# Kernel optimization log

Measured on AMD Instinct MI355X. Metric: run time of the kernel, lower is better.

The kernel has to match this reference:

```python
import math
import jax, jax.numpy as jnp
import numpy as np

B, T, H, E = 2, 1024, 8, 64
M = 128   # nb_features
W = 64    # local_context
NEG = -1e24

def _gaussian_orthogonal(m, d, rng):
    # Orthogonal random features (ortho_scaling=0: rows scaled by chi norms)
    blocks = []
    for _ in range(math.ceil(m / d)):
        q, _ = np.linalg.qr(rng.standard_normal((d, d)))
        blocks.append(q.T)
    mat = np.concatenate(blocks, 0)[:m]
    multiplier = np.linalg.norm(rng.standard_normal((m, d)), axis=1)
    return (multiplier[:, None] * mat).astype(np.float32)

def setup_inputs() -> dict:
    key = jax.random.key(0)
    kq, kk, kv = jax.random.split(key, 3)
    rng = np.random.default_rng(0)
    return {
        'query': jax.random.normal(kq, (B, T, H, E), jnp.float32),
        'key':   jax.random.normal(kk, (B, T, H, E), jnp.float32),
        'value': jax.random.normal(kv, (B, T, H, E), jnp.float32),
        'projection_matrix': jnp.asarray(_gaussian_orthogonal(M, E, rng)),
    }

def _performer_features(x, proj, is_query, temp):
    # x: (b,h,s,e), proj: (m,e). FAVOR+ positive softmax features with
    # the stabilizer returned separately as a log scale.
    normalizer = math.sqrt(temp)
    data_dash = jnp.einsum('bhse,me->bhsm', normalizer * x, proj)
    diag = 0.5 * temp * jnp.sum(x * x, axis=-1, keepdims=True)
    log_feat = data_dash - diag                      # (b,h,s,m)
    if is_query:
        stab = jax.lax.stop_gradient(jnp.max(log_feat, axis=-1, keepdims=True))      # (b,h,s,1)
    else:
        stab = jax.lax.stop_gradient(jnp.max(log_feat, axis=(-2, -1), keepdims=True))  # (b,h,1,1)
    prime = (M ** -0.5) * jnp.exp(log_feat - stab)
    return prime, stab

def reference(query, key, value, projection_matrix):
    q = jnp.transpose(query, (0, 2, 1, 3))   # (b,h,t,e)
    k = jnp.transpose(key, (0, 2, 1, 3))
    v = jnp.transpose(value, (0, 2, 1, 3))
    temp = 1.0 / math.sqrt(E)

    q_prime, q_log_scale = _performer_features(q, projection_matrix, True, temp)
    k_prime, k_log_scale = _performer_features(k, projection_matrix, False, temp)
    prime_log_scale = q_log_scale + k_log_scale        # (b,h,t,1)

    # low-rank Performer terms (non-causal linear attention)
    qk1 = jnp.einsum('bhtm,bhm->bht', q_prime, k_prime.sum(axis=2))
    kv = jnp.einsum('bhsm,bhsd->bhmd', k_prime, v)
    qkv = jnp.einsum('bhtm,bhmd->bhtd', q_prime, kv)

    # banded local attention: query t attends keys t - W//2 + j, j in [0,W)
    local_idx = jnp.arange(T)[:, None] - W // 2 + jnp.arange(W)[None, :]  # (t,w)
    valid = (local_idx >= 0) & (local_idx < T)
    cidx = jnp.clip(local_idx, 0, T - 1)

    k_win = jnp.take(k, cidx, axis=2)                  # (b,h,t,w,e)
    QK = temp * jnp.einsum('bhte,bhtwe->bhtw', q, k_win)
    QK = jnp.where(valid, QK, NEG)

    kp_win = jnp.take(k_prime, cidx, axis=2)           # (b,h,t,w,m)
    dots_prime = jnp.einsum('bhtm,bhtwm->bhtw', q_prime, kp_win)
    dots_prime = jnp.where(valid, dots_prime, 0.0)

    # log-space normalization combining exact local mass and low-rank remainder
    QK_lse = jax.nn.logsumexp(QK, axis=-1, keepdims=True)
    dps = dots_prime.sum(axis=-1, keepdims=True)
    lr_log_norm = jnp.log(jnp.clip(qk1[..., None] - dps, 1e-24, None)) + prime_log_scale
    log_norm = jnp.logaddexp(QK_lse, lr_log_norm)
    prime_scale = jnp.exp(prime_log_scale - log_norm)
    dots = jnp.exp(QK - log_norm) - dots_prime * prime_scale  # (b,h,t,w)

    v_win = jnp.take(v, cidx, axis=2)                  # (b,h,t,w,d)
    out_local = jnp.einsum('bhtw,bhtwd->bhtd', dots, v_win)
    out = out_local + qkv * prime_scale
    return jnp.transpose(out, (0, 2, 1, 3))            # (b,t,h,d)
```

## Files before the change

kernel.cpp:

```cpp
#include <hip/hip_runtime.h>

#define TT 1024
#define HH 8
#define EE 64
#define MM 128
#define NBH 16

#define NORMALIZER 0.35355339059327379f
#define RSQRT_M    0.08838834764831845f
#define TEMP       0.125f
#define NEGINF     -1e24f

typedef __attribute__((ext_vector_type(8))) short short8v;
typedef __attribute__((ext_vector_type(4))) float f32x4;
#define MFMA_BF16 __builtin_amdgcn_mfma_f32_16x16x32_bf16

#define OFF_QP    0u
#define OFF_KF    8388608u
#define OFF_KVP   16777216u
#define OFF_KV    25165824u
#define OFF_KSUM  25690112u
#define OFF_QSTAB 25698304u
#define OFF_KSUMP 25763840u
#define OFF_WTMAX 25894912u

__device__ __forceinline__ unsigned short f2bf(float x) {
  unsigned u = __float_as_uint(x);
  u += 0x7FFFu + ((u >> 16) & 1u);
  return (unsigned short)(u >> 16);
}
__device__ __forceinline__ float bf2f(unsigned short h) {
  return __uint_as_float(((unsigned)h) << 16);
}
__device__ __forceinline__ void f2bf2(float x, unsigned short& hi, unsigned short& lo) {
  hi = f2bf(x);
  lo = f2bf(x - bf2f(hi));
}
__device__ __forceinline__ short8v ldfrag(const short* buf, int ld, int rowbase,
                                          int kbase, int lane) {
  return *(const short8v*)&buf[(rowbase + (lane & 15)) * ld + kbase + ((lane >> 4) << 3)];
}

__global__ __launch_bounds__(256, 2) void feat_kernel(
    const float* __restrict__ Q, const float* __restrict__ K,
    const float* __restrict__ proj,
    float* __restrict__ qp, float* __restrict__ kf,
    float* __restrict__ qstab, float* __restrict__ wtmax)
{
  __shared__ float xsT[64][65];
  __shared__ float Mh[64][4];

  const int bid  = blockIdx.x;
  const int path = bid >> 8;
  const int bh   = (bid >> 4) & 15;
  const int rt   = bid & 15;
  const int b = bh >> 3, h = bh & 7;
  const int t0 = rt << 6;
  const int tid = threadIdx.x;

  const float* x = path ? K : Q;
  const float* xbase = x + (((size_t)b * TT * HH + h) << 6);
#pragma unroll
  for (int it = 0; it < 4; ++it) {
    const int idx = (it << 8) + tid;
    const int r = idx >> 4, c = (idx & 15) << 2;
    const float4 f4 = *(const float4*)&xbase[(size_t)(t0 + r) * 512 + c];
    xsT[c + 0][r] = f4.x; xsT[c + 1][r] = f4.y;
    xsT[c + 2][r] = f4.z; xsT[c + 3][r] = f4.w;
  }
  __syncthreads();

  const int lane = tid & 63;
  const int w = __builtin_amdgcn_readfirstlane(tid >> 6);
  float xv[64];
  float diag = 0.f;
#pragma unroll
  for (int c = 0; c < 64; ++c) { xv[c] = xsT[c][lane]; diag = fmaf(xv[c], xv[c], diag); }
  diag *= 0.0625f;

  float lf[32];
  float mx = -3e30f;
  const int mbase = w << 5;
  for (int mm = 0; mm < 32; ++mm) {
    const float* pr = proj + ((mbase + mm) << 6);
    float a0 = 0.f, a1 = 0.f;
#pragma unroll
    for (int c = 0; c < 64; c += 2) {
      a0 = fmaf(xv[c], pr[c], a0);
      a1 = fmaf(xv[c + 1], pr[c + 1], a1);
    }
    const float v = fmaf(NORMALIZER, a0 + a1, -diag);
    lf[mm] = v;
    mx = fmaxf(mx, v);
  }
  Mh[lane][w] = mx;
  __syncthreads();
  const float m0 = fmaxf(fmaxf(Mh[lane][0], Mh[lane][1]), fmaxf(Mh[lane][2], Mh[lane][3]));

  float ov[32];
  if (path == 0) {
#pragma unroll
    for (int mm = 0; mm < 32; ++mm) ov[mm] = RSQRT_M * __expf(lf[mm] - m0);
    if (w == 0) qstab[(size_t)bh * TT + t0 + lane] = m0;
  } else {
#pragma unroll
    for (int mm = 0; mm < 32; ++mm) ov[mm] = __expf(lf[mm]);
    if (w == 0) {
      float bm = m0;
#pragma unroll
      for (int off = 1; off < 64; off <<= 1) bm = fmaxf(bm, __shfl_xor(bm, off));
      if (lane == 0) wtmax[(bh << 4) + rt] = bm;
    }
  }
  float* dst = (path ? kf : qp) + (((size_t)bh * TT + t0 + lane) << 7) + mbase;
#pragma unroll
  for (int q4 = 0; q4 < 8; ++q4)
    *(float4*)&dst[q4 << 2] =
        make_float4(ov[q4 * 4], ov[q4 * 4 + 1], ov[q4 * 4 + 2], ov[q4 * 4 + 3]);
}

__global__ __launch_bounds__(256, 2) void kv_partial(
    const float* __restrict__ V, const float* __restrict__ kf,
    float* __restrict__ kvp, float* __restrict__ ksump)
{
  __shared__ __align__(16) float smem[64 * 132 + 64 * 68];
  float (*kp_s)[132] = (float(*)[132])smem;
  float (*vs)[68] = (float(*)[68])(smem + 64 * 132);

  const int bid = blockIdx.x;
  const int bh = bid >> 4, st = bid & 15;
  const int b = bh >> 3, h = bh & 7;
  const int tid = threadIdx.x;
  const int row0 = st << 6;
  const size_t base_kf = ((size_t)bh * TT + row0) << 7;

#pragma unroll
  for (int it = 0; it < 8; ++it) {
    const int idx = (it << 10) + (tid << 2);
    const int r = idx >> 7, c = idx & 127;
    *(float4*)&kp_s[r][c] = *(const float4*)&kf[base_kf + idx];
  }
#pragma unroll
  for (int it = 0; it < 4; ++it) {
    const int idx = (it << 10) + (tid << 2);
    const int r = idx >> 6, c = idx & 63;
    *(float4*)&vs[r][c] = *(const float4*)(V + ((((size_t)b * TT + row0 + r) * HH + h) << 6) + c);
  }
  __syncthreads();

  if (tid < 128) {
    float s = 0.f;
    for (int ss = 0; ss < 64; ++ss) s += kp_s[ss][tid];
    ksump[(bid << 7) + tid] = s;
  }

  const int h2 = tid >> 7;
  const int m0 = ((tid & 127) >> 3) << 3;
  const int d0 = (tid & 7) << 3;
  float acc[8][8];
#pragma unroll
  for (int i = 0; i < 8; ++i)
#pragma unroll
    for (int j = 0; j < 8; ++j) acc[i][j] = 0.f;

  const int s0 = h2 << 5;
  for (int ss = s0; ss < s0 + 32; ++ss) {
    const float4 k0v = *(const float4*)&kp_s[ss][m0];
    const float4 k1v = *(const float4*)&kp_s[ss][m0 + 4];
    const float4 v0v = *(const float4*)&vs[ss][d0];
    const float4 v1v = *(const float4*)&vs[ss][d0 + 4];
    const float km[8] = {k0v.x,k0v.y,k0v.z,k0v.w,k1v.x,k1v.y,k1v.z,k1v.w};
    const float vd[8] = {v0v.x,v0v.y,v0v.z,v0v.w,v1v.x,v1v.y,v1v.z,v1v.w};
#pragma unroll
    for (int i = 0; i < 8; ++i)
#pragma unroll
      for (int j = 0; j < 8; ++j) acc[i][j] = fmaf(km[i], vd[j], acc[i][j]);
  }
  __syncthreads();
  float (*kvm)[68] = (float(*)[68])smem;
  if (h2 == 0) {
#pragma unroll
    for (int i = 0; i < 8; ++i)
#pragma unroll
      for (int j = 0; j < 8; ++j) kvm[m0 + i][d0 + j] = acc[i][j];
  }
  __syncthreads();
  if (h2 == 1) {
#pragma unroll
    for (int i = 0; i < 8; ++i)
#pragma unroll
      for (int j = 0; j < 8; ++j) kvm[m0 + i][d0 + j] += acc[i][j];
  }
  __syncthreads();
  float* kvb = kvp + ((size_t)bid << 13);
#pragma unroll
  for (int it = 0; it < 8; ++it) {
    const int idx = (it << 10) + (tid << 2);
    const int m = idx >> 6, d = idx & 63;
    *(float4*)&kvb[idx] = make_float4(kvm[m][d], kvm[m][d + 1], kvm[m][d + 2], kvm[m][d + 3]);
  }
}

__global__ __launch_bounds__(256, 4) void kv_reduce(
    const float* __restrict__ kvp, const float* __restrict__ ksump,
    const float* __restrict__ wtmax,
    float* __restrict__ kv, float* __restrict__ ksum)
{
  const int bid = blockIdx.x;
  const int tid = threadIdx.x;
  if (bid < 128) {
    const int g = (bid << 10) + (tid << 2);
    const int bh = g >> 13, idx = g & 8191;
    float kml = wtmax[bh << 4];
#pragma unroll
    for (int i = 1; i < 16; ++i) kml = fmaxf(kml, wtmax[(bh << 4) + i]);
    const float scale = RSQRT_M * __expf(-kml);
    float4 s = make_float4(0.f, 0.f, 0.f, 0.f);
#pragma unroll
    for (int p = 0; p < 16; ++p) {
      const float4 v = *(const float4*)&kvp[((((size_t)bh << 4) + p) << 13) + idx];
      s.x += v.x; s.y += v.y; s.z += v.z; s.w += v.w;
    }
    s.x *= scale; s.y *= scale; s.z *= scale; s.w *= scale;
    *(float4*)&kv[((size_t)bh << 13) + idx] = s;
  } else {
    const int g = ((bid - 128) << 8) + tid;
    const int bh = g >> 7, m = g & 127;
    float kml = wtmax[bh << 4];
#pragma unroll
    for (int i = 1; i < 16; ++i) kml = fmaxf(kml, wtmax[(bh << 4) + i]);
    const float scale = RSQRT_M * __expf(-kml);
    float s = 0.f;
#pragma unroll
    for (int p = 0; p < 16; ++p) s += ksump[(((bh << 4) + p) << 7) + m];
    ksum[(bh << 7) + m] = s * scale;
  }
}

__global__ __launch_bounds__(256, 2) void band_kernel(
    const float* __restrict__ Q, const float* __restrict__ K,
    const float* __restrict__ V,
    const float* __restrict__ qp, const float* __restrict__ kp,
    const float* __restrict__ kv, const float* __restrict__ ksum,
    const float* __restrict__ qstab, const float* __restrict__ wtmax,
    float* __restrict__ out)
{
  __shared__ __align__(16) short smem[39168];
  __shared__ float pls_s[64];
  short* const qA_hi = smem;
  short* const qA_lo = smem + 4608;
  short* const B_hi  = smem + 9216;
  short* const B_lo  = smem + 18432;
  short* const kvT_hi = smem + 27648;
  short* const kvT_lo = smem + 33408;
  short* const VT_hi  = smem;
  short* const VT_lo  = smem + 8704;
  short* const dots_hi = smem + 17408;
  short* const dots_lo = smem + 26112;

  const int g = blockIdx.x;
  const int lg = ((g & 7) << 5) | (g >> 3);
  const int bh = lg >> 4, tile = lg & 15;
  const int b = bh >> 3, h = bh & 7;
  const int t0 = tile << 6;
  const int k0 = t0 - 32;
  const int tid = threadIdx.x;
  const int lane = tid & 63;
  const int wq = __builtin_amdgcn_readfirstlane(tid >> 6);

  float kml = wtmax[bh << 4];
#pragma unroll
  for (int i = 1; i < 16; ++i) kml = fmaxf(kml, wtmax[(bh << 4) + i]);
  const float kscale = RSQRT_M * __expf(-kml);

  const float* Qbase = Q + (((size_t)b * TT * HH + h) << 6);
  const float* Kbase = K + (((size_t)b * TT * HH + h) << 6);
  const float* Vbase = V + (((size_t)b * TT * HH + h) << 6);
  const float* qpb = qp + (((size_t)bh * TT) << 7);
  const float* kpb = kp + (((size_t)bh * TT) << 7);
  const float* kvb = kv + ((size_t)bh << 13);
  const float* ksb = ksum + (bh << 7);

#pragma unroll
  for (int it = 0; it < 4; ++it) {
    const int idx = (it << 8) + tid;
    const int r = idx >> 4, cc = (idx & 15) << 2;
    const float4 v = *(const float4*)&Qbase[(size_t)(t0 + r) * 512 + cc];
    short4 hi4, lo4;
    f2bf2(v.x, (unsigned short&)hi4.x, (unsigned short&)lo4.x);
    f2bf2(v.y, (unsigned short&)hi4.y, (unsigned short&)lo4.y);
    f2bf2(v.z, (unsigned short&)hi4.z, (unsigned short&)lo4.z);
    f2bf2(v.w, (unsigned short&)hi4.w, (unsigned short&)lo4.w);
    *(short4*)&qA_hi[r * 72 + cc] = hi4;
    *(short4*)&qA_lo[r * 72 + cc] = lo4;
  }
#pragma unroll
  for (int it = 0; it < 8; ++it) {
    const int idx = (it << 8) + tid;
    const int r = idx >> 4, cc = (idx & 15) << 2;
    const int tg = min(max(k0 + r, 0), TT - 1);
    const float4 v = *(const float4*)&Kbase[(size_t)tg * 512 + cc];
    short4 hi4, lo4;
    f2bf2(v.x, (unsigned short&)hi4.x, (unsigned short&)lo4.x);
    f2bf2(v.y, (unsigned short&)hi4.y, (unsigned short&)lo4.y);
    f2bf2(v.z, (unsigned short&)hi4.z, (unsigned short&)lo4.z);
    f2bf2(v.w, (unsigned short&)hi4.w, (unsigned short&)lo4.w);
    *(short4*)&B_hi[r * 72 + cc] = hi4;
    *(short4*)&B_lo[r * 72 + cc] = lo4;
  }
  if (tid < 64) pls_s[tid] = qstab[(size_t)bh * TT + t0 + tid] + kml;
  __syncthreads();

  f32x4 C1[8];
#pragma unroll
  for (int nt = 0; nt < 8; ++nt) C1[nt] = (f32x4){0.f, 0.f, 0.f, 0.f};
  {
    const short8v qh0 = ldfrag(qA_hi, 72, wq << 4, 0, lane);
    const short8v qh1 = ldfrag(qA_hi, 72, wq << 4, 32, lane);
    const short8v ql0 = ldfrag(qA_lo, 72, wq << 4, 0, lane);
    const short8v ql1 = ldfrag(qA_lo, 72, wq << 4, 32, lane);
#pragma unroll
    for (int nt = 0; nt < 8; ++nt) {
      const short8v bh0 = ldfrag(B_hi, 72, nt << 4, 0, lane);
      const short8v bh1 = ldfrag(B_hi, 72, nt << 4, 32, lane);
      C1[nt] = MFMA_BF16(qh0, bh0, C1[nt], 0, 0, 0);
      C1[nt] = MFMA_BF16(qh1, bh1, C1[nt], 0, 0, 0);
      C1[nt] = MFMA_BF16(qh0, ldfrag(B_lo, 72, nt << 4, 0, lane), C1[nt], 0, 0, 0);
      C1[nt] = MFMA_BF16(qh1, ldfrag(B_lo, 72, nt << 4, 32, lane), C1[nt], 0, 0, 0);
      C1[nt] = MFMA_BF16(ql0, bh0, C1[nt], 0, 0, 0);
      C1[nt] = MFMA_BF16(ql1, bh1, C1[nt], 0, 0, 0);
    }
  }
  __syncthreads();

  f32x4 C2[8], C3[5];
#pragma unroll
  for (int nt = 0; nt < 8; ++nt) C2[nt] = (f32x4){0.f, 0.f, 0.f, 0.f};
#pragma unroll
  for (int nt = 0; nt < 5; ++nt) C3[nt] = (f32x4){0.f, 0.f, 0.f, 0.f};

#pragma unroll 1
  for (int c = 0; c < 2; ++c) {
    const int co = c << 6;
#pragma unroll
    for (int it = 0; it < 4; ++it) {
      const int idx = (it << 8) + tid;
      const int r = idx >> 4, cc = (idx & 15) << 2;
      const float4 v = *(const float4*)&qpb[((size_t)(t0 + r) << 7) + co + cc];
      short4 hi4, lo4;
      f2bf2(v.x, (unsigned short&)hi4.x, (unsigned short&)lo4.x);
      f2bf2(v.y, (unsigned short&)hi4.y, (unsigned short&)lo4.y);
      f2bf2(v.z, (unsigned short&)hi4.z, (unsigned short&)lo4.z);
      f2bf2(v.w, (unsigned short&)hi4.w, (unsigned short&)lo4.w);
      *(short4*)&qA_hi[r * 72 + cc] = hi4;
      *(short4*)&qA_lo[r * 72 + cc] = lo4;
    }
#pragma unroll
    for (int it = 0; it < 8; ++it) {
      const int idx = (it << 8) + tid;
      const int r = idx >> 4, cc = (idx & 15) << 2;
      const int tg = min(max(k0 + r, 0), TT - 1);
      const float4 v = *(const float4*)&kpb[((size_t)tg << 7) + co + cc];
      short4 hi4, lo4;
      f2bf2(v.x, (unsigned short&)hi4.x, (unsigned short&)lo4.x);
      f2bf2(v.y, (unsigned short&)hi4.y, (unsigned short&)lo4.y);
      f2bf2(v.z, (unsigned short&)hi4.z, (unsigned short&)lo4.z);
      f2bf2(v.w, (unsigned short&)hi4.w, (unsigned short&)lo4.w);
      *(short4*)&B_hi[r * 72 + cc] = hi4;
      *(short4*)&B_lo[r * 72 + cc] = lo4;
    }
    {
      const int mloc = tid >> 2, db = (tid & 3) << 4;
      const float4* kr = (const float4*)(kvb + ((co + mloc) << 6) + db);
#pragma unroll
      for (int i2 = 0; i2 < 4; ++i2) {
        const float4 v = kr[i2];
        const int dr = db + (i2 << 2);
        unsigned short hs, ls;
        f2bf2(v.x, hs, ls); kvT_hi[(dr + 0) * 72 + mloc] = hs; kvT_lo[(dr + 0) * 72 + mloc] = ls;
        f2bf2(v.y, hs, ls); kvT_hi[(dr + 1) * 72 + mloc] = hs; kvT_lo[(dr + 1) * 72 + mloc] = ls;
        f2bf2(v.z, hs, ls); kvT_hi[(dr + 2) * 72 + mloc] = hs; kvT_lo[(dr + 2) * 72 + mloc] = ls;
        f2bf2(v.w, hs, ls); kvT_hi[(dr + 3) * 72 + mloc] = hs; kvT_lo[(dr + 3) * 72 + mloc] = ls;
      }
    }
    if (tid < 64) {
      const float x = ksb[co + tid];
      unsigned short hs, ls;
      f2bf2(x, hs, ls);
      kvT_hi[64 * 72 + tid] = hs;
      kvT_hi[65 * 72 + tid] = ls;
      kvT_lo[64 * 72 + tid] = 0;
      kvT_lo[65 * 72 + tid] = 0;
    }
    __syncthreads();

    const short8v ph0 = ldfrag(qA_hi, 72, wq << 4, 0, lane);
    const short8v ph1 = ldfrag(qA_hi, 72, wq << 4, 32, lane);
    const short8v pl0 = ldfrag(qA_lo, 72, wq << 4, 0, lane);
    const short8v pl1 = ldfrag(qA_lo, 72, wq << 4, 32, lane);
#pragma unroll
    for (int nt = 0; nt < 8; ++nt) {
      const short8v bh0 = ldfrag(B_hi, 72, nt << 4, 0, lane);
      const short8v bh1 = ldfrag(B_hi, 72, nt << 4, 32, lane);
      C2[nt] = MFMA_BF16(ph0, bh0, C2[nt], 0, 0, 0);
      C2[nt] = MFMA_BF16(ph1, bh1, C2[nt], 0, 0, 0);
      C2[nt] = MFMA_BF16(ph0, ldfrag(B_lo, 72, nt << 4, 0, lane), C2[nt], 0, 0, 0);
      C2[nt] = MFMA_BF16(ph1, ldfrag(B_lo, 72, nt << 4, 32, lane), C2[nt], 0, 0, 0);
      C2[nt] = MFMA_BF16(pl0, bh0, C2[nt], 0, 0, 0);
      C2[nt] = MFMA_BF16(pl1, bh1, C2[nt], 0, 0, 0);
    }
#pragma unroll
    for (int nt = 0; nt < 5; ++nt) {
      const short8v kh0 = ldfrag(kvT_hi, 72, nt << 4, 0, lane);
      const short8v kh1 = ldfrag(kvT_hi, 72, nt << 4, 32, lane);
      C3[nt] = MFMA_BF16(ph0, kh0, C3[nt], 0, 0, 0);
      C3[nt] = MFMA_BF16(ph1, kh1, C3[nt], 0, 0, 0);
      C3[nt] = MFMA_BF16(ph0, ldfrag(kvT_lo, 72, nt << 4, 0, lane), C3[nt], 0, 0, 0);
      C3[nt] = MFMA_BF16(ph1, ldfrag(kvT_lo, 72, nt << 4, 32, lane), C3[nt], 0, 0, 0);
      C3[nt] = MFMA_BF16(pl0, kh0, C3[nt], 0, 0, 0);
      C3[nt] = MFMA_BF16(pl1, kh1, C3[nt], 0, 0, 0);
    }
    __syncthreads();
  }

  {
    const int jl = tid >> 1, db = (tid & 1) << 5;
    const int tg = min(max(k0 + jl, 0), TT - 1);
    const float4* vr = (const float4*)&Vbase[(size_t)tg * 512 + db];
#pragma unroll
    for (int i2 = 0; i2 < 8; ++i2) {
      const float4 v = vr[i2];
      const int dr = db + (i2 << 2);
      unsigned short hs, ls;
      f2bf2(v.x, hs, ls); VT_hi[(dr + 0) * 136 + jl] = hs; VT_lo[(dr + 0) * 136 + jl] = ls;
      f2bf2(v.y, hs, ls); VT_hi[(dr + 1) * 136 + jl] = hs; VT_lo[(dr + 1) * 136 + jl] = ls;
      f2bf2(v.z, hs, ls); VT_hi[(dr + 2) * 136 + jl] = hs; VT_lo[(dr + 2) * 136 + jl] = ls;
      f2bf2(v.w, hs, ls); VT_hi[(dr + 3) * 136 + jl] = hs; VT_lo[(dr + 3) * 136 + jl] = ls;
    }
  }

  float psr[4];
  const int lrow = (lane >> 4) << 2;
  const int lcol = lane & 15;
#pragma unroll
  for (int r = 0; r < 4; ++r) {
    const int ql = (wq << 4) + lrow + r;
    float qkt[8], dpt[8];
    float mx = -3e30f;
#pragma unroll
    for (int nt = 0; nt < 8; ++nt) {
      const int kr = (nt << 4) + lcol;
      const int j = kr - ql;
      const int gk = k0 + kr;
      const bool vv = (j >= 0) && (j < 64) && (gk >= 0) && (gk < TT);
      qkt[nt] = vv ? TEMP * C1[nt][r] : NEGINF;
      dpt[nt] = vv ? kscale * C2[nt][r] : 0.f;
      mx = fmaxf(mx, qkt[nt]);
    }
    mx = fmaxf(mx, __shfl_xor(mx, 1));
    mx = fmaxf(mx, __shfl_xor(mx, 2));
    mx = fmaxf(mx, __shfl_xor(mx, 4));
    mx = fmaxf(mx, __shfl_xor(mx, 8));
    float se = 0.f, dps = 0.f;
#pragma unroll
    for (int nt = 0; nt < 8; ++nt) {
      se += __expf(qkt[nt] - mx);
      dps += dpt[nt];
    }
    se += __shfl_xor(se, 1); se += __shfl_xor(se, 2);
    se += __shfl_xor(se, 4); se += __shfl_xor(se, 8);
    dps += __shfl_xor(dps, 1); dps += __shfl_xor(dps, 2);
    dps += __shfl_xor(dps, 4); dps += __shfl_xor(dps, 8);
    const float qk1 = __shfl(C3[4][r], lane & 48) + __shfl(C3[4][r], (lane & 48) + 1);

    const float pls = pls_s[ql];
    const float lse = mx + __logf(se);
    const float lr = fmaxf(qk1 - dps, 1e-24f);
    const float lrl = __logf(lr) + pls;
    const float aa = fmaxf(lse, lrl), bb = fminf(lse, lrl);
    const float ln = aa + log1pf(__expf(bb - aa));
    psr[r] = __expf(pls - ln);
#pragma unroll
    for (int nt = 0; nt < 8; ++nt) {
      const float d = __expf(qkt[nt] - ln) - dpt[nt] * psr[r];
      unsigned short hs, ls;
      f2bf2(d, hs, ls);
      dots_hi[ql * 136 + (nt << 4) + lcol] = hs;
      dots_lo[ql * 136 + (nt << 4) + lcol] = ls;
    }
  }
  __syncthreads();

  f32x4 D4[4];
#pragma unroll
  for (int nt = 0; nt < 4; ++nt) D4[nt] = (f32x4){0.f, 0.f, 0.f, 0.f};
#pragma unroll
  for (int kk = 0; kk < 4; ++kk) {
    const short8v adh = ldfrag(dots_hi, 136, wq << 4, kk << 5, lane);
    const short8v adl = ldfrag(dots_lo, 136, wq << 4, kk << 5, lane);
#pragma unroll
    for (int nt = 0; nt < 4; ++nt) {
      const short8v vh = ldfrag(VT_hi, 136, nt << 4, kk << 5, lane);
      D4[nt] = MFMA_BF16(adh, vh, D4[nt], 0, 0, 0);
      D4[nt] = MFMA_BF16(adh, ldfrag(VT_lo, 136, nt << 4, kk << 5, lane), D4[nt], 0, 0, 0);
      D4[nt] = MFMA_BF16(adl, vh, D4[nt], 0, 0, 0);
    }
  }
#pragma unroll
  for (int nt = 0; nt < 4; ++nt) {
#pragma unroll
    for (int r = 0; r < 4; ++r) {
      const int ql = (wq << 4) + lrow + r;
      const float val = D4[nt][r] + C3[nt][r] * psr[r];
      out[((((size_t)b * TT + t0 + ql) * HH + h) << 6) + (nt << 4) + lcol] = val;
    }
  }
}

extern "C" void kernel_launch(void* const* d_in, const int* in_sizes, int n_in,
                              void* d_out, int out_size, void* d_ws, size_t ws_size,
                              hipStream_t stream) {
  (void)in_sizes; (void)n_in; (void)out_size; (void)ws_size;
  const float* Q    = (const float*)d_in[0];
  const float* K    = (const float*)d_in[1];
  const float* V    = (const float*)d_in[2];
  const float* proj = (const float*)d_in[3];
  float* out = (float*)d_out;
  char* ws = (char*)d_ws;

  float* qp    = (float*)(ws + OFF_QP);
  float* kf    = (float*)(ws + OFF_KF);
  float* kvp   = (float*)(ws + OFF_KVP);
  float* kv    = (float*)(ws + OFF_KV);
  float* ksum  = (float*)(ws + OFF_KSUM);
  float* qstab = (float*)(ws + OFF_QSTAB);
  float* ksump = (float*)(ws + OFF_KSUMP);
  float* wtmax = (float*)(ws + OFF_WTMAX);

  feat_kernel<<<512, 256, 0, stream>>>(Q, K, proj, qp, kf, qstab, wtmax);
  kv_partial<<<256, 256, 0, stream>>>(V, kf, kvp, ksump);
  kv_reduce<<<136, 256, 0, stream>>>(kvp, ksump, wtmax, kv, ksum);
  band_kernel<<<256, 256, 0, stream>>>(Q, K, V, qp, kf, kv, ksum, qstab, wtmax, out);
}
```

Baseline: 68.22 us.

## Fuse kv_partial into feature kernel and precompute bf16 hi/lo operands

Merges the kv_partial stage into the key path of the feature kernel, so K features go straight from registers into shared memory without a global round trip. The feature kernel also writes Q, K, Q', K' and transposed V as split bf16 hi/lo arrays, and kv_reduce now emits a transposed bf16 kv plus ksum. The band kernel then loads these pre-converted operands directly, dropping its repeated float-to-bf16 conversions and taking Q fragments straight from global memory. The cost is a larger feature kernel with more shared memory, extra global writes, and a kv_reduce with only 16 blocks.

```diff
diff --git a/kernel.cpp b/kernel.cpp
--- a/kernel.cpp
+++ b/kernel.cpp
@@ -15,14 +15,22 @@
 typedef __attribute__((ext_vector_type(4))) float f32x4;
 #define MFMA_BF16 __builtin_amdgcn_mfma_f32_16x16x32_bf16
 
-#define OFF_QP    0u
-#define OFF_KF    8388608u
-#define OFF_KVP   16777216u
-#define OFF_KV    25165824u
-#define OFF_KSUM  25690112u
-#define OFF_QSTAB 25698304u
-#define OFF_KSUMP 25763840u
-#define OFF_WTMAX 25894912u
+#define OFF_QPH   0u
+#define OFF_QPL   4194304u
+#define OFF_KPH   8388608u
+#define OFF_KPL   12582912u
+#define OFF_Q16H  16777216u
+#define OFF_Q16L  18874368u
+#define OFF_K16H  20971520u
+#define OFF_K16L  23068672u
+#define OFF_VTH   25165824u
+#define OFF_VTL   27262976u
+#define OFF_KVP   29360128u
+#define OFF_KSUMP 37748736u
+#define OFF_WTMAX 37879808u
+#define OFF_QSTAB 37880832u
+#define OFF_KVT_H 37946368u
+#define OFF_KVT_L 38216704u
 
 __device__ __forceinline__ unsigned short f2bf(float x) {
   unsigned u = __float_as_uint(x);
@@ -38,22 +46,23 @@
 }
 __device__ __forceinline__ short8v ldfrag(const short* buf, int ld, int rowbase,
                                           int kbase, int lane) {
-  return *(const short8v*)&buf[(rowbase + (lane & 15)) * ld + kbase + ((lane >> 4) << 3)];
+  return *(const short8v*)&buf[(size_t)(rowbase + (lane & 15)) * ld + kbase + ((lane >> 4) << 3)];
 }
 
 __global__ __launch_bounds__(256, 2) void feat_kernel(
     const float* __restrict__ Q, const float* __restrict__ K,
-    const float* __restrict__ proj,
-    float* __restrict__ qp, float* __restrict__ kf,
-    float* __restrict__ qstab, float* __restrict__ wtmax)
+    const float* __restrict__ V, const float* __restrict__ proj,
+    char* __restrict__ ws)
 {
   __shared__ float xsT[64][65];
   __shared__ float Mh[64][4];
+  __shared__ __align__(16) float smem2[64 * 132 + 64 * 68];
 
   const int bid  = blockIdx.x;
-  const int path = bid >> 8;
-  const int bh   = (bid >> 4) & 15;
-  const int rt   = bid & 15;
+  const int path = bid & 1;
+  const int rest = bid >> 1;
+  const int bh   = rest >> 4;
+  const int rt   = rest & 15;
   const int b = bh >> 3, h = bh & 7;
   const int t0 = rt << 6;
   const int tid = threadIdx.x;
@@ -101,7 +110,7 @@
   if (path == 0) {
 #pragma unroll
     for (int mm = 0; mm < 32; ++mm) ov[mm] = RSQRT_M * __expf(lf[mm] - m0);
-    if (w == 0) qstab[(size_t)bh * TT + t0 + lane] = m0;
+    if (w == 0) ((float*)(ws + OFF_QSTAB))[(size_t)bh * TT + t0 + lane] = m0;
   } else {
 #pragma unroll
     for (int mm = 0; mm < 32; ++mm) ov[mm] = __expf(lf[mm]);
@@ -109,64 +118,87 @@
       float bm = m0;
 #pragma unroll
       for (int off = 1; off < 64; off <<= 1) bm = fmaxf(bm, __shfl_xor(bm, off));
-      if (lane == 0) wtmax[(bh << 4) + rt] = bm;
-    }
-  }
-  float* dst = (path ? kf : qp) + (((size_t)bh * TT + t0 + lane) << 7) + mbase;
+      if (lane == 0) ((float*)(ws + OFF_WTMAX))[(bh << 4) + rt] = bm;
+    }
+  }
+
+  {
+    short* fh = (short*)(ws + (path ? OFF_KPH : OFF_QPH)) +
+                (((size_t)bh * TT + t0 + lane) << 7) + mbase;
+    short* fl = (short*)(ws + (path ? OFF_KPL : OFF_QPL)) +
+                (((size_t)bh * TT + t0 + lane) << 7) + mbase;
+#pragma unroll
+    for (int q4 = 0; q4 < 8; ++q4) {
+      short4 h4, l4;
+      f2bf2(ov[q4 * 4 + 0], (unsigned short&)h4.x, (unsigned short&)l4.x);
+      f2bf2(ov[q4 * 4 + 1], (unsigned short&)h4.y, (unsigned short&)l4.y);
+      f2bf2(ov[q4 * 4 + 2], (unsigned short&)h4.z, (unsigned short&)l4.z);
+      f2bf2(ov[q4 * 4 + 3], (unsigned short&)h4.w, (unsigned short&)l4.w);
+      *(short4*)&fh[q4 << 2] = h4;
+      *(short4*)&fl[q4 << 2] = l4;
+    }
+  }
+
+  {
+    short* xh = (short*)(ws + (path ? OFF_K16H : OFF_Q16H)) + ((size_t)bh * TT + t0) * 64;
+    short* xl = (short*)(ws + (path ? OFF_K16L : OFF_Q16L)) + ((size_t)bh * TT + t0) * 64;
+#pragma unroll
+    for (int it = 0; it < 2; ++it) {
+      const int gg = (it << 8) + tid;
+      const int r = gg >> 3, c8 = (gg & 7) << 3;
+      short4 h0, h1, l0, l1;
+      f2bf2(xsT[c8 + 0][r], (unsigned short&)h0.x, (unsigned short&)l0.x);
+      f2bf2(xsT[c8 + 1][r], (unsigned short&)h0.y, (unsigned short&)l0.y);
+      f2bf2(xsT[c8 + 2][r], (unsigned short&)h0.z, (unsigned short&)l0.z);
+      f2bf2(xsT[c8 + 3][r], (unsigned short&)h0.w, (unsigned short&)l0.w);
+      f2bf2(xsT[c8 + 4][r], (unsigned short&)h1.x, (unsigned short&)l1.x);
+      f2bf2(xsT[c8 + 5][r], (unsigned short&)h1.y, (unsigned short&)l1.y);
+      f2bf2(xsT[c8 + 6][r], (unsigned short&)h1.z, (unsigned short&)l1.z);
+      f2bf2(xsT[c8 + 7][r], (unsigned short&)h1.w, (unsigned short&)l1.w);
+      *(short4*)&xh[r * 64 + c8 + 0] = h0;
+      *(short4*)&xh[r * 64 + c8 + 4] = h1;
+      *(short4*)&xl[r * 64 + c8 + 0] = l0;
+      *(short4*)&xl[r * 64 + c8 + 4] = l1;
+    }
+  }
+
+  if (path == 0) return;
+
+  float (*kp_s)[132] = (float(*)[132])smem2;
+  float (*vs)[68] = (float(*)[68])(smem2 + 64 * 132);
+
 #pragma unroll
   for (int q4 = 0; q4 < 8; ++q4)
-    *(float4*)&dst[q4 << 2] =
+    *(float4*)&kp_s[lane][mbase + (q4 << 2)] =
         make_float4(ov[q4 * 4], ov[q4 * 4 + 1], ov[q4 * 4 + 2], ov[q4 * 4 + 3]);
-}
-
-__global__ __launch_bounds__(256, 2) void kv_partial(
-    const float* __restrict__ V, const float* __restrict__ kf,
-    float* __restrict__ kvp, float* __restrict__ ksump)
-{
-  __shared__ __align__(16) float smem[64 * 132 + 64 * 68];
-  float (*kp_s)[132] = (float(*)[132])smem;
-  float (*vs)[68] = (float(*)[68])(smem + 64 * 132);
-
-  const int bid = blockIdx.x;
-  const int bh = bid >> 4, st = bid & 15;
-  const int b = bh >> 3, h = bh & 7;
-  const int tid = threadIdx.x;
-  const int row0 = st << 6;
-  const size_t base_kf = ((size_t)bh * TT + row0) << 7;
-
-#pragma unroll
-  for (int it = 0; it < 8; ++it) {
-    const int idx = (it << 10) + (tid << 2);
-    const int r = idx >> 7, c = idx & 127;
-    *(float4*)&kp_s[r][c] = *(const float4*)&kf[base_kf + idx];
-  }
+
+  const float* Vbase = V + (((size_t)b * TT * HH + h) << 6);
 #pragma unroll
   for (int it = 0; it < 4; ++it) {
     const int idx = (it << 10) + (tid << 2);
     const int r = idx >> 6, c = idx & 63;
-    *(float4*)&vs[r][c] = *(const float4*)(V + ((((size_t)b * TT + row0 + r) * HH + h) << 6) + c);
+    *(float4*)&vs[r][c] = *(const float4*)&Vbase[(size_t)(t0 + r) * 512 + c];
   }
   __syncthreads();
 
   if (tid < 128) {
     float s = 0.f;
     for (int ss = 0; ss < 64; ++ss) s += kp_s[ss][tid];
-    ksump[(bid << 7) + tid] = s;
+    ((float*)(ws + OFF_KSUMP))[(rest << 7) + tid] = s;
   }
 
   const int h2 = tid >> 7;
-  const int m0 = ((tid & 127) >> 3) << 3;
+  const int m0i = ((tid & 127) >> 3) << 3;
   const int d0 = (tid & 7) << 3;
   float acc[8][8];
 #pragma unroll
   for (int i = 0; i < 8; ++i)
 #pragma unroll
     for (int j = 0; j < 8; ++j) acc[i][j] = 0.f;
-
   const int s0 = h2 << 5;
   for (int ss = s0; ss < s0 + 32; ++ss) {
-    const float4 k0v = *(const float4*)&kp_s[ss][m0];
-    const float4 k1v = *(const float4*)&kp_s[ss][m0 + 4];
+    const float4 k0v = *(const float4*)&kp_s[ss][m0i];
+    const float4 k1v = *(const float4*)&kp_s[ss][m0i + 4];
     const float4 v0v = *(const float4*)&vs[ss][d0];
     const float4 v1v = *(const float4*)&vs[ss][d0 + 4];
     const float km[8] = {k0v.x,k0v.y,k0v.z,k0v.w,k1v.x,k1v.y,k1v.z,k1v.w};
@@ -176,23 +208,40 @@
 #pragma unroll
       for (int j = 0; j < 8; ++j) acc[i][j] = fmaf(km[i], vd[j], acc[i][j]);
   }
-  __syncthreads();
-  float (*kvm)[68] = (float(*)[68])smem;
+
+  {
+    short* vh = (short*)(ws + OFF_VTH) + (size_t)bh * 64 * TT;
+    short* vl = (short*)(ws + OFF_VTL) + (size_t)bh * 64 * TT;
+    const int d = tid >> 2, jg = (tid & 3) << 4;
+#pragma unroll
+    for (int j0 = 0; j0 < 16; j0 += 4) {
+      short4 h4, l4;
+      f2bf2(vs[jg + j0 + 0][d], (unsigned short&)h4.x, (unsigned short&)l4.x);
+      f2bf2(vs[jg + j0 + 1][d], (unsigned short&)h4.y, (unsigned short&)l4.y);
+      f2bf2(vs[jg + j0 + 2][d], (unsigned short&)h4.z, (unsigned short&)l4.z);
+      f2bf2(vs[jg + j0 + 3][d], (unsigned short&)h4.w, (unsigned short&)l4.w);
+      *(short4*)&vh[(size_t)d * TT + t0 + jg + j0] = h4;
+      *(short4*)&vl[(size_t)d * TT + t0 + jg + j0] = l4;
+    }
+  }
+  __syncthreads();
+
+  float (*kvm)[68] = (float(*)[68])smem2;
   if (h2 == 0) {
 #pragma unroll
     for (int i = 0; i < 8; ++i)
 #pragma unroll
-      for (int j = 0; j < 8; ++j) kvm[m0 + i][d0 + j] = acc[i][j];
+      for (int j = 0; j < 8; ++j) kvm[m0i + i][d0 + j] = acc[i][j];
   }
   __syncthreads();
   if (h2 == 1) {
 #pragma unroll
     for (int i = 0; i < 8; ++i)
 #pragma unroll
-      for (int j = 0; j < 8; ++j) kvm[m0 + i][d0 + j] += acc[i][j];
-  }
-  __syncthreads();
-  float* kvb = kvp + ((size_t)bid << 13);
+      for (int j = 0; j < 8; ++j) kvm[m0i + i][d0 + j] += acc[i][j];
+  }
+  __syncthreads();
+  float* kvb = (float*)(ws + OFF_KVP) + ((size_t)rest << 13);
 #pragma unroll
   for (int it = 0; it < 8; ++it) {
     const int idx = (it << 10) + (tid << 2);
@@ -201,60 +250,77 @@
   }
 }
 
-__global__ __launch_bounds__(256, 4) void kv_reduce(
-    const float* __restrict__ kvp, const float* __restrict__ ksump,
-    const float* __restrict__ wtmax,
-    float* __restrict__ kv, float* __restrict__ ksum)
+__global__ __launch_bounds__(256, 2) void kv_reduce(char* __restrict__ ws)
 {
-  const int bid = blockIdx.x;
+  __shared__ float kvT_s[64 * 130];
+  const int bh = blockIdx.x;
   const int tid = threadIdx.x;
-  if (bid < 128) {
-    const int g = (bid << 10) + (tid << 2);
-    const int bh = g >> 13, idx = g & 8191;
-    float kml = wtmax[bh << 4];
-#pragma unroll
-    for (int i = 1; i < 16; ++i) kml = fmaxf(kml, wtmax[(bh << 4) + i]);
-    const float scale = RSQRT_M * __expf(-kml);
-    float4 s = make_float4(0.f, 0.f, 0.f, 0.f);
-#pragma unroll
-    for (int p = 0; p < 16; ++p) {
-      const float4 v = *(const float4*)&kvp[((((size_t)bh << 4) + p) << 13) + idx];
-      s.x += v.x; s.y += v.y; s.z += v.z; s.w += v.w;
-    }
-    s.x *= scale; s.y *= scale; s.z *= scale; s.w *= scale;
-    *(float4*)&kv[((size_t)bh << 13) + idx] = s;
-  } else {
-    const int g = ((bid - 128) << 8) + tid;
-    const int bh = g >> 7, m = g & 127;
-    float kml = wtmax[bh << 4];
-#pragma unroll
-    for (int i = 1; i < 16; ++i) kml = fmaxf(kml, wtmax[(bh << 4) + i]);
-    const float scale = RSQRT_M * __expf(-kml);
-    float s = 0.f;
-#pragma unroll
-    for (int p = 0; p < 16; ++p) s += ksump[(((bh << 4) + p) << 7) + m];
-    ksum[(bh << 7) + m] = s * scale;
+  const float* wtmax = (const float*)(ws + OFF_WTMAX);
+  float kml = wtmax[bh << 4];
+#pragma unroll
+  for (int i = 1; i < 16; ++i) kml = fmaxf(kml, wtmax[(bh << 4) + i]);
+  const float scale = RSQRT_M * __expf(-kml);
+
+  const float* kvp = (const float*)(ws + OFF_KVP);
+  const int m = tid >> 1, dh = (tid & 1) << 5;
+  float s[32];
+#pragma unroll
+  for (int i = 0; i < 32; ++i) s[i] = 0.f;
+#pragma unroll
+  for (int p = 0; p < 16; ++p) {
+    const float* base = kvp + ((((size_t)(bh << 4) + p) << 13) | ((size_t)m << 6)) + dh;
+#pragma unroll
+    for (int i = 0; i < 8; ++i) {
+      const float4 v = *(const float4*)&base[i << 2];
+      s[i * 4 + 0] += v.x; s[i * 4 + 1] += v.y; s[i * 4 + 2] += v.z; s[i * 4 + 3] += v.w;
+    }
+  }
+#pragma unroll
+  for (int i = 0; i < 32; ++i) kvT_s[(dh + i) * 130 + m] = s[i] * scale;
+
+  float ks = 0.f;
+  if (tid < 128) {
+    const float* ksump = (const float*)(ws + OFF_KSUMP);
+#pragma unroll
+    for (int p = 0; p < 16; ++p) ks += ksump[(((bh << 4) + p) << 7) + tid];
+    ks *= scale;
+  }
+  __syncthreads();
+
+  short* kh = (short*)(ws + OFF_KVT_H) + (size_t)bh * 66 * 128;
+  short* kl = (short*)(ws + OFF_KVT_L) + (size_t)bh * 66 * 128;
+  const int d = tid >> 2, mg = (tid & 3) << 5;
+#pragma unroll
+  for (int j0 = 0; j0 < 32; j0 += 4) {
+    short4 h4, l4;
+    f2bf2(kvT_s[d * 130 + mg + j0 + 0], (unsigned short&)h4.x, (unsigned short&)l4.x);
+    f2bf2(kvT_s[d * 130 + mg + j0 + 1], (unsigned short&)h4.y, (unsigned short&)l4.y);
+    f2bf2(kvT_s[d * 130 + mg + j0 + 2], (unsigned short&)h4.z, (unsigned short&)l4.z);
+    f2bf2(kvT_s[d * 130 + mg + j0 + 3], (unsigned short&)h4.w, (unsigned short&)l4.w);
+    *(short4*)&kh[d * 128 + mg + j0] = h4;
+    *(short4*)&kl[d * 128 + mg + j0] = l4;
+  }
+  if (tid < 128) {
+    unsigned short hs, ls;
+    f2bf2(ks, hs, ls);
+    kh[64 * 128 + tid] = hs;
+    kh[65 * 128 + tid] = ls;
+    kl[64 * 128 + tid] = 0;
+    kl[65 * 128 + tid] = 0;
   }
 }
 
 __global__ __launch_bounds__(256, 2) void band_kernel(
-    const float* __restrict__ Q, const float* __restrict__ K,
-    const float* __restrict__ V,
-    const float* __restrict__ qp, const float* __restrict__ kp,
-    const float* __restrict__ kv, const float* __restrict__ ksum,
-    const float* __restrict__ qstab, const float* __restrict__ wtmax,
-    float* __restrict__ out)
+    char* __restrict__ ws, float* __restrict__ out)
 {
-  __shared__ __align__(16) short smem[39168];
+  __shared__ __align__(16) short smem[34816];
   __shared__ float pls_s[64];
-  short* const qA_hi = smem;
-  short* const qA_lo = smem + 4608;
-  short* const B_hi  = smem + 9216;
-  short* const B_lo  = smem + 18432;
-  short* const kvT_hi = smem + 27648;
-  short* const kvT_lo = smem + 33408;
-  short* const VT_hi  = smem;
-  short* const VT_lo  = smem + 8704;
+  short* const B_hi   = smem;
+  short* const B_lo   = smem + 9216;
+  short* const kvT_hi = smem + 18432;
+  short* const kvT_lo = smem + 24192;
+  short* const VT_hi   = smem;
+  short* const VT_lo   = smem + 8704;
   short* const dots_hi = smem + 17408;
   short* const dots_lo = smem + 26112;
 
@@ -268,57 +334,46 @@
   const int lane = tid & 63;
   const int wq = __builtin_amdgcn_readfirstlane(tid >> 6);
 
+  const float* wtmax = (const float*)(ws + OFF_WTMAX);
   float kml = wtmax[bh << 4];
 #pragma unroll
   for (int i = 1; i < 16; ++i) kml = fmaxf(kml, wtmax[(bh << 4) + i]);
   const float kscale = RSQRT_M * __expf(-kml);
 
-  const float* Qbase = Q + (((size_t)b * TT * HH + h) << 6);
-  const float* Kbase = K + (((size_t)b * TT * HH + h) << 6);
-  const float* Vbase = V + (((size_t)b * TT * HH + h) << 6);
-  const float* qpb = qp + (((size_t)bh * TT) << 7);
-  const float* kpb = kp + (((size_t)bh * TT) << 7);
-  const float* kvb = kv + ((size_t)bh << 13);
-  const float* ksb = ksum + (bh << 7);
-
-#pragma unroll
-  for (int it = 0; it < 4; ++it) {
-    const int idx = (it << 8) + tid;
-    const int r = idx >> 4, cc = (idx & 15) << 2;
-    const float4 v = *(const float4*)&Qbase[(size_t)(t0 + r) * 512 + cc];
-    short4 hi4, lo4;
-    f2bf2(v.x, (unsigned short&)hi4.x, (unsigned short&)lo4.x);
-    f2bf2(v.y, (unsigned short&)hi4.y, (unsigned short&)lo4.y);
-    f2bf2(v.z, (unsigned short&)hi4.z, (unsigned short&)lo4.z);
-    f2bf2(v.w, (unsigned short&)hi4.w, (unsigned short&)lo4.w);
-    *(short4*)&qA_hi[r * 72 + cc] = hi4;
-    *(short4*)&qA_lo[r * 72 + cc] = lo4;
-  }
+  const short* q16h = (const short*)(ws + OFF_Q16H) + ((size_t)bh * TT + t0) * 64;
+  const short* q16l = (const short*)(ws + OFF_Q16L) + ((size_t)bh * TT + t0) * 64;
+  const short* qph  = (const short*)(ws + OFF_QPH) + (((size_t)bh * TT + t0) << 7);
+  const short* qpl  = (const short*)(ws + OFF_QPL) + (((size_t)bh * TT + t0) << 7);
+  const short* k16h = (const short*)(ws + OFF_K16H) + (size_t)bh * TT * 64;
+  const short* k16l = (const short*)(ws + OFF_K16L) + (size_t)bh * TT * 64;
+  const short* kphg = (const short*)(ws + OFF_KPH) + ((size_t)bh * TT << 7);
+  const short* kplg = (const short*)(ws + OFF_KPL) + ((size_t)bh * TT << 7);
+  const short* kvth = (const short*)(ws + OFF_KVT_H) + (size_t)bh * 66 * 128;
+  const short* kvtl = (const short*)(ws + OFF_KVT_L) + (size_t)bh * 66 * 128;
+  const short* vth  = (const short*)(ws + OFF_VTH) + (size_t)bh * 64 * TT;
+  const short* vtl  = (const short*)(ws + OFF_VTL) + (size_t)bh * 64 * TT;
+
+  if (tid < 64)
+    pls_s[tid] = ((const float*)(ws + OFF_QSTAB))[(size_t)bh * TT + t0 + tid] + kml;
+
 #pragma unroll
   for (int it = 0; it < 8; ++it) {
-    const int idx = (it << 8) + tid;
-    const int r = idx >> 4, cc = (idx & 15) << 2;
+    const int gg = (it << 8) + tid;
+    const int r = gg >> 4, c4 = (gg & 15) << 2;
     const int tg = min(max(k0 + r, 0), TT - 1);
-    const float4 v = *(const float4*)&Kbase[(size_t)tg * 512 + cc];
-    short4 hi4, lo4;
-    f2bf2(v.x, (unsigned short&)hi4.x, (unsigned short&)lo4.x);
-    f2bf2(v.y, (unsigned short&)hi4.y, (unsigned short&)lo4.y);
-    f2bf2(v.z, (unsigned short&)hi4.z, (unsigned short&)lo4.z);
-    f2bf2(v.w, (unsigned short&)hi4.w, (unsigned short&)lo4.w);
-    *(short4*)&B_hi[r * 72 + cc] = hi4;
-    *(short4*)&B_lo[r * 72 + cc] = lo4;
-  }
-  if (tid < 64) pls_s[tid] = qstab[(size_t)bh * TT + t0 + tid] + kml;
+    *(short4*)&B_hi[r * 72 + c4] = *(const short4*)&k16h[(size_t)tg * 64 + c4];
+    *(short4*)&B_lo[r * 72 + c4] = *(const short4*)&k16l[(size_t)tg * 64 + c4];
+  }
   __syncthreads();
 
   f32x4 C1[8];
 #pragma unroll
   for (int nt = 0; nt < 8; ++nt) C1[nt] = (f32x4){0.f, 0.f, 0.f, 0.f};
   {
-    const short8v qh0 = ldfrag(qA_hi, 72, wq << 4, 0, lane);
-    const short8v qh1 = ldfrag(qA_hi, 72, wq << 4, 32, lane);
-    const short8v ql0 = ldfrag(qA_lo, 72, wq << 4, 0, lane);
-    const short8v ql1 = ldfrag(qA_lo, 72, wq << 4, 32, lane);
+    const short8v qh0 = ldfrag(q16h, 64, wq << 4, 0, lane);
+    const short8v qh1 = ldfrag(q16h, 64, wq << 4, 32, lane);
+    const short8v ql0 = ldfrag(q16l, 64, wq << 4, 0, lane);
+    const short8v ql1 = ldfrag(q16l, 64, wq << 4, 32, lane);
 #pragma unroll
     for (int nt = 0; nt < 8; ++nt) {
       const short8v bh0 = ldfrag(B_hi, 72, nt << 4, 0, lane);
@@ -331,7 +386,6 @@
       C1[nt] = MFMA_BF16(ql1, bh1, C1[nt], 0, 0, 0);
     }
   }
-  __syncthreads();
 
   f32x4 C2[8], C3[5];
 #pragma unroll
@@ -342,62 +396,33 @@
 #pragma unroll 1
   for (int c = 0; c < 2; ++c) {
     const int co = c << 6;
+    __syncthreads();
+#pragma unroll
+    for (int it = 0; it < 8; ++it) {
+      const int gg = (it << 8) + tid;
+      const int r = gg >> 4, c4 = (gg & 15) << 2;
+      const int tg = min(max(k0 + r, 0), TT - 1);
+      *(short4*)&B_hi[r * 72 + c4] = *(const short4*)&kphg[((size_t)tg << 7) + co + c4];
+      *(short4*)&B_lo[r * 72 + c4] = *(const short4*)&kplg[((size_t)tg << 7) + co + c4];
+    }
 #pragma unroll
     for (int it = 0; it < 4; ++it) {
-      const int idx = (it << 8) + tid;
-      const int r = idx >> 4, cc = (idx & 15) << 2;
-      const float4 v = *(const float4*)&qpb[((size_t)(t0 + r) << 7) + co + cc];
-      short4 hi4, lo4;
-      f2bf2(v.x, (unsigned short&)hi4.x, (unsigned short&)lo4.x);
-      f2bf2(v.y, (unsigned short&)hi4.y, (unsigned short&)lo4.y);
-      f2bf2(v.z, (unsigned short&)hi4.z, (unsigned short&)lo4.z);
-      f2bf2(v.w, (unsigned short&)hi4.w, (unsigned short&)lo4.w);
-      *(short4*)&qA_hi[r * 72 + cc] = hi4;
-      *(short4*)&qA_lo[r * 72 + cc] = lo4;
-    }
-#pragma unroll
-    for (int it = 0; it < 8; ++it) {
-      const int idx = (it << 8) + tid;
-      const int r = idx >> 4, cc = (idx & 15) << 2;
-      const int tg = min(max(k0 + r, 0), TT - 1);
-      const float4 v = *(const float4*)&kpb[((size_t)tg << 7) + co + cc];
-      short4 hi4, lo4;
-      f2bf2(v.x, (unsigned short&)hi4.x, (unsigned short&)lo4.x);
-      f2bf2(v.y, (unsigned short&)hi4.y, (unsigned short&)lo4.y);
-      f2bf2(v.z, (unsigned short&)hi4.z, (unsigned short&)lo4.z);
-      f2bf2(v.w, (unsigned short&)hi4.w, (unsigned short&)lo4.w);
-      *(short4*)&B_hi[r * 72 + cc] = hi4;
-      *(short4*)&B_lo[r * 72 + cc] = lo4;
-    }
-    {
-      const int mloc = tid >> 2, db = (tid & 3) << 4;
-      const float4* kr = (const float4*)(kvb + ((co + mloc) << 6) + db);
-#pragma unroll
-      for (int i2 = 0; i2 < 4; ++i2) {
-        const float4 v = kr[i2];
-        const int dr = db + (i2 << 2);
-        unsigned short hs, ls;
-        f2bf2(v.x, hs, ls); kvT_hi[(dr + 0) * 72 + mloc] = hs; kvT_lo[(dr + 0) * 72 + mloc] = ls;
-        f2bf2(v.y, hs, ls); kvT_hi[(dr + 1) * 72 + mloc] = hs; kvT_lo[(dr + 1) * 72 + mloc] = ls;
-        f2bf2(v.z, hs, ls); kvT_hi[(dr + 2) * 72 + mloc] = hs; kvT_lo[(dr + 2) * 72 + mloc] = ls;
-        f2bf2(v.w, hs, ls); kvT_hi[(dr + 3) * 72 + mloc] = hs; kvT_lo[(dr + 3) * 72 + mloc] = ls;
-      }
-    }
-    if (tid < 64) {
-      const float x = ksb[co + tid];
-      unsigned short hs, ls;
-      f2bf2(x, hs, ls);
-      kvT_hi[64 * 72 + tid] = hs;
-      kvT_hi[65 * 72 + tid] = ls;
-      kvT_lo[64 * 72 + tid] = 0;
-      kvT_lo[65 * 72 + tid] = 0;
+      const int gg = (it << 8) + tid;
+      const int r = gg >> 4, c4 = (gg & 15) << 2;
+      *(short4*)&kvT_hi[r * 72 + c4] = *(const short4*)&kvth[(size_t)r * 128 + co + c4];
+      *(short4*)&kvT_lo[r * 72 + c4] = *(const short4*)&kvtl[(size_t)r * 128 + co + c4];
+    }
+    if (tid < 128) {
+      const int r = 64 + (tid >> 6), mm = tid & 63;
+      kvT_hi[r * 72 + mm] = kvth[(size_t)r * 128 + co + mm];
+      kvT_lo[r * 72 + mm] = 0;
     }
     __syncthreads();
 
-    const short8v ph0 = ldfrag(qA_hi, 72, wq << 4, 0, lane);
-    const short8v ph1 = ldfrag(qA_hi, 72, wq << 4, 32, lane);
-    const short8v pl0 = ldfrag(qA_lo, 72, wq << 4, 0, lane);
-    const short8v pl1 = ldfrag(qA_lo, 72, wq << 4, 32, lane);
+    const short8v ph0 = ldfrag(qph, 128, wq << 4, co + 0, lane);
+    const short8v ph1 = ldfrag(qph, 128, wq << 4, co + 32, lane);
+    const short8v pl0 = ldfrag(qpl, 128, wq << 4, co + 0, lane);
+    const short8v pl1 = ldfrag(qpl, 128, wq << 4, co + 32, lane);
 #pragma unroll
     for (int nt = 0; nt < 8; ++nt) {
       const short8v bh0 = ldfrag(B_hi, 72, nt << 4, 0, lane);
@@ -420,23 +445,30 @@
       C3[nt] = MFMA_BF16(pl0, kh0, C3[nt], 0, 0, 0);
       C3[nt] = MFMA_BF16(pl1, kh1, C3[nt], 0, 0, 0);
     }
-    __syncthreads();
-  }
-
-  {
-    const int jl = tid >> 1, db = (tid & 1) << 5;
-    const int tg = min(max(k0 + jl, 0), TT - 1);
-    const float4* vr = (const float4*)&Vbase[(size_t)tg * 512 + db];
-#pragma unroll
-    for (int i2 = 0; i2 < 8; ++i2) {
-      const float4 v = vr[i2];
-      const int dr = db + (i2 << 2);
-      unsigned short hs, ls;
-      f2bf2(v.x, hs, ls); VT_hi[(dr + 0) * 136 + jl] = hs; VT_lo[(dr + 0) * 136 + jl] = ls;
-      f2bf2(v.y, hs, ls); VT_hi[(dr + 1) * 136 + jl] = hs; VT_lo[(dr + 1) * 136 + jl] = ls;
-      f2bf2(v.z, hs, ls); VT_hi[(dr + 2) * 136 + jl] = hs; VT_lo[(dr + 2) * 136 + jl] = ls;
-      f2bf2(v.w, hs, ls); VT_hi[(dr + 3) * 136 + jl] = hs; VT_lo[(dr + 3) * 136 + jl] = ls;
-    }
+  }
+  __syncthreads();
+
+#pragma unroll
+  for (int it = 0; it < 8; ++it) {
+    const int gg = (it << 8) + tid;
+    const int d = gg >> 5, j4 = (gg & 31) << 2;
+    const int jj = k0 + j4;
+    short4 h4, l4;
+    if (jj >= 0 && jj <= TT - 4) {
+      h4 = *(const short4*)&vth[(size_t)d * TT + jj];
+      l4 = *(const short4*)&vtl[(size_t)d * TT + jj];
+    } else {
+      const int j0c = min(max(jj + 0, 0), TT - 1);
+      const int j1c = min(max(jj + 1, 0), TT - 1);
+      const int j2c = min(max(jj + 2, 0), TT - 1);
+      const int j3c = min(max(jj + 3, 0), TT - 1);
+      h4.x = vth[(size_t)d * TT + j0c]; l4.x = vtl[(size_t)d * TT + j0c];
+      h4.y = vth[(size_t)d * TT + j1c]; l4.y = vtl[(size_t)d * TT + j1c];
+      h4.z = vth[(size_t)d * TT + j2c]; l4.z = vtl[(size_t)d * TT + j2c];
+      h4.w = vth[(size_t)d * TT + j3c]; l4.w = vtl[(size_t)d * TT + j3c];
+    }
+    *(short4*)&VT_hi[d * 136 + j4] = h4;
+    *(short4*)&VT_lo[d * 136 + j4] = l4;
   }
 
   float psr[4];
@@ -528,17 +560,7 @@
   float* out = (float*)d_out;
   char* ws = (char*)d_ws;
 
-  float* qp    = (float*)(ws + OFF_QP);
-  float* kf    = (float*)(ws + OFF_KF);
-  float* kvp   = (float*)(ws + OFF_KVP);
-  float* kv    = (float*)(ws + OFF_KV);
-  float* ksum  = (float*)(ws + OFF_KSUM);
-  float* qstab = (float*)(ws + OFF_QSTAB);
-  float* ksump = (float*)(ws + OFF_KSUMP);
-  float* wtmax = (float*)(ws + OFF_WTMAX);
-
-  feat_kernel<<<512, 256, 0, stream>>>(Q, K, proj, qp, kf, qstab, wtmax);
-  kv_partial<<<256, 256, 0, stream>>>(V, kf, kvp, ksump);
-  kv_reduce<<<136, 256, 0, stream>>>(kvp, ksump, wtmax, kv, ksum);
-  band_kernel<<<256, 256, 0, stream>>>(Q, K, V, qp, kf, kv, ksum, qstab, wtmax, out);
-}
+  feat_kernel<<<512, 256, 0, stream>>>(Q, K, V, proj, ws);
+  kv_reduce<<<16, 256, 0, stream>>>(ws);
+  band_kernel<<<256, 256, 0, stream>>>(ws, out);
+}
```

Result: slower. 86.18 us (+26.3%).
